# Optimization experiments

Hardware: AMD Instinct MI355X
Metric: run time of the kernel (lower is better)

## Reference

```python
import jax, jax.numpy as jnp
import numpy as np

NUM_HEADS = 1


def setup_inputs() -> dict:
    key = jax.random.key(0)
    k1, k2, k3 = jax.random.split(key, 3)
    B, C, H, W = 32, 1024, 32, 32
    x = jax.random.normal(k1, (B, C, H, W), dtype=jnp.float32)
    w_qkv = jax.random.normal(k2, (3 * C, C), dtype=jnp.float32) * (C ** -0.5)
    w_proj = jax.random.normal(k3, (C, C), dtype=jnp.float32) * (C ** -0.5)
    b_proj = jnp.zeros((C,), dtype=jnp.float32)
    return {"x": x, "w_qkv": w_qkv, "w_proj": w_proj, "b_proj": b_proj}


def reference(x, w_qkv, w_proj, b_proj):
    B, C, H, W = x.shape
    nh = NUM_HEADS
    hd = C // nh
    S = H * W
    # 1x1 conv (no bias) == channel matmul
    qkv = jnp.einsum('bchw,oc->bohw', x, w_qkv)          # [B, 3C, H, W]
    qkv = qkv.reshape(B * nh, 3 * hd, S)
    q, k, v = jnp.split(qkv, 3, axis=1)                   # each [B*nh, hd, S]
    scale = hd ** -0.25
    attn = jax.nn.softmax(
        jnp.einsum('bct,bcs->bts', q * scale, k * scale), axis=-1)  # [B*nh, S, S]
    # faithful to source einsum 'bts,bcs->bts': sums v over channel dim only
    h = attn * jnp.sum(v, axis=1, keepdims=True)          # [B*nh, S, S]
    h = h.reshape(B, nh * S, H, W)                        # requires nh*S == C
    out = jnp.einsum('bchw,oc->bohw', h, w_proj) + b_proj[None, :, None, None]
    return out + x
```

## Files before the change

### kernel.cpp

```cpp
#include <hip/hip_runtime.h>
#include <hip/hip_bf16.h>
#include <stdint.h>


typedef __attribute__((ext_vector_type(8))) short short8;
typedef __attribute__((ext_vector_type(4))) float f32x4;

__device__ __forceinline__ short f2b(float f) {
    __hip_bfloat16 h = __float2bfloat16(f);
    return *reinterpret_cast<short*>(&h);
}
__device__ __forceinline__ float b2f(short s) {
    __hip_bfloat16 h;
    *reinterpret_cast<short*>(&h) = s;
    return __bfloat162float(h);
}

#define GLOAD16(gp, lp) __builtin_amdgcn_global_load_lds(                      \
    (const __attribute__((address_space(1))) unsigned int*)(gp),               \
    (__attribute__((address_space(3))) unsigned int*)(lp), 16, 0, 0)

#define WAITV4 asm volatile("s_waitcnt vmcnt(4)" ::: "memory")
#define WAITV0 asm volatile("s_waitcnt vmcnt(0)" ::: "memory")
#define WAITL0 asm volatile("s_waitcnt lgkmcnt(0)" ::: "memory")
#define BAR()  { asm volatile("" ::: "memory"); __builtin_amdgcn_s_barrier(); \
                 asm volatile("" ::: "memory"); }

__global__ void k_wvsum(const float* __restrict__ wqkv, float* __restrict__ wvsum) {
    int c = blockIdx.x * 256 + threadIdx.x;
    int o0 = blockIdx.y * 32;
    float s = 0.f;
    const float* p = wqkv + (size_t)(2048 + o0) * 1024 + c;
    #pragma unroll 8
    for (int o = 0; o < 32; ++o) s += p[(size_t)o * 1024];
    atomicAdd(&wvsum[c], s);
}

__global__ void k_cvt(const float* __restrict__ in, short* __restrict__ out) {
    int i = (blockIdx.x * 256 + threadIdx.x) * 4;
    #pragma unroll
    for (int j = 0; j < 4; ++j) out[i + j] = f2b(in[i + j]);
}

__global__ void k_xpose(const float* __restrict__ x, const float* __restrict__ wvsum,
                        short* __restrict__ xT, float* __restrict__ vsum) {
    __shared__ float tile[32][33];
    __shared__ float ps[8][32];
    int b = blockIdx.z;
    int s0 = blockIdx.x * 32, c0 = blockIdx.y * 32;
    int tx = threadIdx.x, ty = threadIdx.y;
    const float* xb = x + ((size_t)b << 20);
    float p = 0.f;
    #pragma unroll
    for (int i = 0; i < 4; ++i) {
        int cl = ty + i * 8;
        float v = xb[(size_t)(c0 + cl) * 1024 + s0 + tx];
        tile[cl][tx] = v;
        p += v * wvsum[c0 + cl];
    }
    ps[ty][tx] = p;
    __syncthreads();
    short* xTb = xT + ((size_t)b << 20);
    #pragma unroll
    for (int i = 0; i < 4; ++i) {
        int sl = ty + i * 8;
        xTb[(size_t)(s0 + sl) * 1024 + c0 + tx] = f2b(tile[tx][sl]);
    }
    if (ty == 0) {
        float s = 0.f;
        #pragma unroll
        for (int i = 0; i < 8; ++i) s += ps[i][tx];
        atomicAdd(&vsum[b * 1024 + s0 + tx], s);
    }
}

template <int MODE, int TM, int TN>
__global__ __launch_bounds__(512, 2)
void k_gemm(const short* __restrict__ A0, size_t strideA, int lda,
            const short* __restrict__ B0, size_t strideB, int ldb,
            void* __restrict__ O0, size_t strideO, int ldo,
            float* __restrict__ Z,
            const float* __restrict__ scale,
            const float* __restrict__ bias,
            const float* __restrict__ xres) {
    __shared__ __align__(16) short As[2 * 256 * 64];
    __shared__ __align__(16) short Bs[2 * 256 * 64];

    constexpr int TPB = TM * TN;
    constexpr int CPX = TPB * 4;
    int wg = blockIdx.x;
    int swz = (wg & 7) * CPX + (wg >> 3);
    int z = swz / TPB;
    int rz = swz - z * TPB;
    int m0 = (rz / TN) * 256, n0 = (rz % TN) * 256;

    int tid = threadIdx.x;
    int wid = tid >> 6, l = tid & 63;
    int wm = wid >> 2, wn = wid & 3;
    int lr = l & 15, lg = l >> 4;

    const short* A = A0 + (size_t)z * strideA;
    const short* Bt = B0 + (size_t)z * strideB;

    int srow = wid * 16 + (l >> 3);
    int scol = ((l & 7) ^ (l >> 3)) * 8;
    const short* gA = A + (size_t)(m0 + srow) * lda + scol;
    const short* gB = Bt + (size_t)(n0 + srow) * ldb + scol;
    char* const ldsA = (char*)As;
    char* const ldsB = (char*)Bs;
    int sdst = wid * 2048;

    auto SA = [&](int buf, int h, int t) __attribute__((always_inline)) {
        const short* g = gA + (size_t)(h * 128) * lda + t * 64;
        char* d = ldsA + buf * 32768 + h * 16384 + sdst;
        GLOAD16(g, d);
        GLOAD16(g + (size_t)8 * lda, d + 1024);
    };
    auto SB = [&](int buf, int h, int t) __attribute__((always_inline)) {
        const short* g = gB + (size_t)(h * 128) * ldb + t * 64;
        char* d = ldsB + buf * 32768 + h * 16384 + sdst;
        GLOAD16(g, d);
        GLOAD16(g + (size_t)8 * ldb, d + 1024);
    };

    int cs0 = ((lg) ^ (lr & 7)) * 16;
    int cs1 = ((4 + lg) ^ (lr & 7)) * 16;
    int arow = (wm * 128 + lr) * 128;
    int brow = (wn * 64 + lr) * 128;

    short8 af[8], bf0[4], bf1[4];
    f32x4 acc[8][4] = {};

    auto RDA = [&](int buf, int mh) __attribute__((always_inline)) {
        const char* p = ldsA + buf * 32768 + arow + mh * 8192;
        #pragma unroll
        for (int mi = 0; mi < 4; ++mi) {
            af[mi * 2]     = *(const short8*)(p + mi * 2048 + cs0);
            af[mi * 2 + 1] = *(const short8*)(p + mi * 2048 + cs1);
        }
    };
    auto RDB = [&](short8* dst, int buf, int nh) __attribute__((always_inline)) {
        const char* p = ldsB + buf * 32768 + brow + nh * 4096;
        #pragma unroll
        for (int ni = 0; ni < 2; ++ni) {
            dst[ni * 2]     = *(const short8*)(p + ni * 2048 + cs0);
            dst[ni * 2 + 1] = *(const short8*)(p + ni * 2048 + cs1);
        }
    };
    auto MMA = [&](const short8* bfp, int mh, int nh) __attribute__((always_inline)) {
        __builtin_amdgcn_s_setprio(1);
        #pragma unroll
        for (int ks = 0; ks < 2; ++ks)
            #pragma unroll
            for (int mi = 0; mi < 4; ++mi)
                #pragma unroll
                for (int ni = 0; ni < 2; ++ni)
                    acc[mh * 4 + mi][nh * 2 + ni] =
                        __builtin_amdgcn_mfma_f32_16x16x32_bf16(
                            af[mi * 2 + ks], bfp[ni * 2 + ks],
                            acc[mh * 4 + mi][nh * 2 + ni], 0, 0, 0);
        __builtin_amdgcn_s_setprio(0);
    };

    SB(0, 0, 0); SB(0, 1, 0); SA(0, 0, 0); SA(0, 1, 0);
    SB(1, 0, 1); SB(1, 1, 1);
    WAITV4;
    BAR();

    for (int t = 0; t < 16; ++t) {
        int b = t & 1;
        RDA(b, 0); RDB(bf0, b, 0);
        if (t < 15) SA(b ^ 1, 0, t + 1);
        BAR(); WAITL0; MMA(bf0, 0, 0); BAR();
        RDB(bf1, b, 1);
        if (t < 15) SA(b ^ 1, 1, t + 1);
        BAR(); WAITL0; MMA(bf1, 0, 1); BAR();
        RDA(b, 1);
        if (t < 14) SB(b, 0, t + 2);
        BAR(); WAITL0; MMA(bf0, 1, 0); BAR();
        if (t < 14) SB(b, 1, t + 2);
        if (t <= 13) { WAITV4; } else if (t == 14) { WAITV0; }
        BAR(); MMA(bf1, 1, 1); BAR();
    }

    int rb = m0 + wm * 128, cb = n0 + wn * 64;
    if (MODE == 0) {
        short* O = (short*)O0 + (size_t)z * strideO;
        #pragma unroll
        for (int mi = 0; mi < 8; ++mi)
            #pragma unroll
            for (int ni = 0; ni < 4; ++ni)
                #pragma unroll
                for (int r = 0; r < 4; ++r)
                    O[(size_t)(rb + mi * 16 + lg * 4 + r) * ldo + cb + ni * 16 + lr] =
                        f2b(acc[mi][ni][r]);
    } else if (MODE == 1) {
        short* O = (short*)O0 + (size_t)z * strideO;
        float* Zb = Z + z * 1024;
        #pragma unroll
        for (int ni = 0; ni < 4; ++ni) {
            float zs = 0.f;
            #pragma unroll
            for (int mi = 0; mi < 8; ++mi)
                #pragma unroll
                for (int r = 0; r < 4; ++r) {
                    float ev = __expf(acc[mi][ni][r] * 0.03125f);
                    O[(size_t)(rb + mi * 16 + lg * 4 + r) * ldo + cb + ni * 16 + lr] = f2b(ev);
                    zs += ev;
                }
            zs += __shfl_xor(zs, 16);
            zs += __shfl_xor(zs, 32);
            if (l < 16) atomicAdd(&Zb[cb + ni * 16 + l], zs);
        }
    } else {
        float* O = (float*)O0 + (size_t)z * strideO;
        const float* xr = xres + (size_t)z * strideO;
        #pragma unroll
        for (int mi = 0; mi < 8; ++mi)
            #pragma unroll
            for (int ni = 0; ni < 4; ++ni)
                #pragma unroll
                for (int r = 0; r < 4; ++r) {
                    int row = rb + mi * 16 + lg * 4 + r;
                    int col = cb + ni * 16 + lr;
                    O[(size_t)row * ldo + col] = acc[mi][ni][r] * scale[z * 1024 + col] +
                                                 bias[row] + xr[(size_t)row * ldo + col];
                }
    }
}

__global__ void k_invz(float* Z) {
    int i = blockIdx.x * 256 + threadIdx.x;
    Z[i] = 1.0f / Z[i];
}

__global__ void k_wpscale(const short* __restrict__ wp_b, const float* __restrict__ invZ,
                          short* __restrict__ wp_s) {
    size_t i8 = ((size_t)blockIdx.x * 256 + threadIdx.x) * 8;
    int b = (int)(i8 >> 20);
    int t0 = (int)(i8 & 1023);
    short8 w = *(const short8*)&wp_b[i8 & 1048575];
    const float* iz = invZ + b * 1024 + t0;
    short8 r;
    #pragma unroll
    for (int j = 0; j < 8; ++j) r[j] = f2b(b2f(w[j]) * iz[j]);
    *(short8*)&wp_s[i8] = r;
}

extern "C" void kernel_launch(void* const* d_in, const int* in_sizes, int n_in,
                              void* d_out, int out_size, void* d_ws, size_t ws_size,
                              hipStream_t stream) {
    const float* x     = (const float*)d_in[0];
    const float* wqkv  = (const float*)d_in[1];
    const float* wproj = (const float*)d_in[2];
    const float* bproj = (const float*)d_in[3];
    float* out = (float*)d_out;

    char* ws = (char*)d_ws;
    size_t off = 0;
    auto alloc = [&](size_t bytes) {
        void* p = ws + off;
        off += (bytes + 255) & ~(size_t)255;
        return p;
    };
    float* wvsum = (float*)alloc(1024 * 4);
    short* wqk_b = (short*)alloc((size_t)2048 * 1024 * 2);
    short* wp_b  = (short*)alloc((size_t)1024 * 1024 * 2);
    short* xT    = (short*)alloc((size_t)32 * 1024 * 1024 * 2);
    short* qkT   = (short*)alloc((size_t)32 * 1024 * 2048 * 2);
    short* attnT = (short*)alloc((size_t)32 * 1024 * 1024 * 2);
    float* vsum  = (float*)alloc(32 * 1024 * 4);
    float* Zbuf  = (float*)alloc(32 * 1024 * 4);

    hipMemsetAsync(wvsum, 0, 1024 * 4, stream);
    hipMemsetAsync(vsum, 0, 32 * 1024 * 4, stream);
    hipMemsetAsync(Zbuf, 0, 32 * 1024 * 4, stream);

    k_wvsum<<<dim3(4, 32), 256, 0, stream>>>(wqkv, wvsum);
    k_cvt<<<2048, 256, 0, stream>>>(wqkv, wqk_b);
    k_cvt<<<1024, 256, 0, stream>>>(wproj, wp_b);
    k_xpose<<<dim3(32, 32, 32), dim3(32, 8), 0, stream>>>(x, wvsum, xT, vsum);

    k_gemm<0, 4, 8><<<1024, 512, 0, stream>>>(
        xT, (size_t)1048576, 1024, wqk_b, 0, 1024,
        qkT, (size_t)2097152, 2048, nullptr, nullptr, nullptr, nullptr);

    k_gemm<1, 4, 4><<<512, 512, 0, stream>>>(
        qkT + 1024, (size_t)2097152, 2048, qkT, (size_t)2097152, 2048,
        attnT, (size_t)1048576, 1024, Zbuf, nullptr, nullptr, nullptr);

    k_invz<<<128, 256, 0, stream>>>(Zbuf);

    short* wp_s = xT;
    k_wpscale<<<16384, 256, 0, stream>>>(wp_b, Zbuf, wp_s);

    k_gemm<2, 4, 4><<<512, 512, 0, stream>>>(
        wp_s, (size_t)1048576, 1024, attnT, (size_t)1048576, 1024,
        out, (size_t)1048576, 1024, nullptr, vsum, bproj, x);
}
```

Measured before the change: 436.5 us.

## Precompute Wk^T Wq product to replace the QKV GEMM with a C×C GEMM

Rewrites the scores q^T k as x^T (Wq^T Wk) x. The weight product M = Wq^T Wk is computed once as a split-K GEMM (8 fp32 partials reduced to bf16), then applied per batch to x. This replaces the 2048-wide QKV projection with a 1024-wide one and stops writing the larger qkT buffer. The GEMM also gains a templated K-iteration count with peeled prologue and epilogue iterations. The extra bf16 rounding of M and of the intermediate product may change numerics slightly.

```diff
diff --git a/kernel.cpp b/kernel.cpp
--- a/kernel.cpp
+++ b/kernel.cpp
@@ -4,6 +4,7 @@
 
 
 typedef __attribute__((ext_vector_type(8))) short short8;
+typedef __attribute__((ext_vector_type(4))) short short4_t;
 typedef __attribute__((ext_vector_type(4))) float f32x4;
 
 __device__ __forceinline__ short f2b(float f) {
@@ -74,7 +75,36 @@
     }
 }
 
-template <int MODE, int TM, int TN>
+__global__ void k_xposew(const float* __restrict__ wqkv, short* __restrict__ WT) {
+    __shared__ float tile[32][33];
+    int w = blockIdx.z;
+    int o0 = blockIdx.x * 32, c0 = blockIdx.y * 32;
+    int tx = threadIdx.x, ty = threadIdx.y;
+    const float* src = wqkv + (size_t)w * 1048576;
+    #pragma unroll
+    for (int i = 0; i < 4; ++i)
+        tile[ty + i * 8][tx] = src[(size_t)(o0 + ty + i * 8) * 1024 + c0 + tx];
+    __syncthreads();
+    short* dst = WT + (size_t)w * 1048576;
+    #pragma unroll
+    for (int i = 0; i < 4; ++i) {
+        int cl = ty + i * 8;
+        dst[(size_t)(c0 + cl) * 1024 + o0 + tx] = f2b(tile[tx][cl]);
+    }
+}
+
+__global__ void k_red8(const float* __restrict__ part, short* __restrict__ MT) {
+    int i4 = (blockIdx.x * 256 + threadIdx.x) * 4;
+    f32x4 s = *(const f32x4*)&part[i4];
+    #pragma unroll
+    for (int z = 1; z < 8; ++z) s += *(const f32x4*)&part[(size_t)z * 1048576 + i4];
+    short4_t r;
+    #pragma unroll
+    for (int j = 0; j < 4; ++j) r[j] = f2b(s[j]);
+    *(short4_t*)&MT[i4] = r;
+}
+
+template <int MODE, int TM, int TN, int NT>
 __global__ __launch_bounds__(512, 2)
 void k_gemm(const short* __restrict__ A0, size_t strideA, int lda,
             const short* __restrict__ B0, size_t strideB, int ldb,
@@ -87,9 +117,9 @@
     __shared__ __align__(16) short Bs[2 * 256 * 64];
 
     constexpr int TPB = TM * TN;
-    constexpr int CPX = TPB * 4;
     int wg = blockIdx.x;
-    int swz = (wg & 7) * CPX + (wg >> 3);
+    int cpx = gridDim.x >> 3;
+    int swz = (wg & 7) * cpx + (wg >> 3);
     int z = swz / TPB;
     int rz = swz - z * TPB;
     int m0 = (rz / TN) * 256, n0 = (rz % TN) * 256;
@@ -163,24 +193,47 @@
     };
 
     SB(0, 0, 0); SB(0, 1, 0); SA(0, 0, 0); SA(0, 1, 0);
-    SB(1, 0, 1); SB(1, 1, 1);
-    WAITV4;
+    if constexpr (NT > 1) {
+        SB(1, 0, 1); SB(1, 1, 1);
+        WAITV4;
+    } else {
+        WAITV0;
+    }
     BAR();
 
-    for (int t = 0; t < 16; ++t) {
+    #pragma unroll 2
+    for (int t = 0; t < NT - 2; ++t) {
         int b = t & 1;
+        RDA(b, 0); RDB(bf0, b, 0); SA(b ^ 1, 0, t + 1);
+        BAR(); WAITL0; MMA(bf0, 0, 0); BAR();
+        RDB(bf1, b, 1); SA(b ^ 1, 1, t + 1);
+        BAR(); WAITL0; MMA(bf1, 0, 1); BAR();
+        RDA(b, 1); SB(b, 0, t + 2);
+        BAR(); WAITL0; MMA(bf0, 1, 0); BAR();
+        SB(b, 1, t + 2); WAITV4;
+        BAR(); MMA(bf1, 1, 1); BAR();
+    }
+    if constexpr (NT > 1) {
+        constexpr int tp = NT - 2;
+        constexpr int b = tp & 1;
+        RDA(b, 0); RDB(bf0, b, 0); SA(b ^ 1, 0, NT - 1);
+        BAR(); WAITL0; MMA(bf0, 0, 0); BAR();
+        RDB(bf1, b, 1); SA(b ^ 1, 1, NT - 1);
+        BAR(); WAITL0; MMA(bf1, 0, 1); BAR();
+        RDA(b, 1);
+        BAR(); WAITL0; MMA(bf0, 1, 0); BAR();
+        WAITV0;
+        BAR(); MMA(bf1, 1, 1); BAR();
+    }
+    {
+        constexpr int b = (NT - 1) & 1;
         RDA(b, 0); RDB(bf0, b, 0);
-        if (t < 15) SA(b ^ 1, 0, t + 1);
         BAR(); WAITL0; MMA(bf0, 0, 0); BAR();
         RDB(bf1, b, 1);
-        if (t < 15) SA(b ^ 1, 1, t + 1);
         BAR(); WAITL0; MMA(bf1, 0, 1); BAR();
         RDA(b, 1);
-        if (t < 14) SB(b, 0, t + 2);
         BAR(); WAITL0; MMA(bf0, 1, 0); BAR();
-        if (t < 14) SB(b, 1, t + 2);
-        if (t <= 13) { WAITV4; } else if (t == 14) { WAITV0; }
-        BAR(); MMA(bf1, 1, 1); BAR();
+        MMA(bf1, 1, 1);
     }
 
     int rb = m0 + wm * 128, cb = n0 + wn * 64;
@@ -212,7 +265,7 @@
             zs += __shfl_xor(zs, 32);
             if (l < 16) atomicAdd(&Zb[cb + ni * 16 + l], zs);
         }
-    } else {
+    } else if (MODE == 2) {
         float* O = (float*)O0 + (size_t)z * strideO;
         const float* xr = xres + (size_t)z * strideO;
         #pragma unroll
@@ -226,6 +279,16 @@
                     O[(size_t)row * ldo + col] = acc[mi][ni][r] * scale[z * 1024 + col] +
                                                  bias[row] + xr[(size_t)row * ldo + col];
                 }
+    } else {
+        float* O = (float*)O0 + (size_t)z * strideO;
+        #pragma unroll
+        for (int mi = 0; mi < 8; ++mi)
+            #pragma unroll
+            for (int ni = 0; ni < 4; ++ni)
+                #pragma unroll
+                for (int r = 0; r < 4; ++r)
+                    O[(size_t)(rb + mi * 16 + lg * 4 + r) * ldo + cb + ni * 16 + lr] =
+                        acc[mi][ni][r];
     }
 }
 
@@ -264,10 +327,12 @@
         return p;
     };
     float* wvsum = (float*)alloc(1024 * 4);
-    short* wqk_b = (short*)alloc((size_t)2048 * 1024 * 2);
     short* wp_b  = (short*)alloc((size_t)1024 * 1024 * 2);
     short* xT    = (short*)alloc((size_t)32 * 1024 * 1024 * 2);
-    short* qkT   = (short*)alloc((size_t)32 * 1024 * 2048 * 2);
+    short* WT    = (short*)alloc((size_t)2 * 1024 * 1024 * 2);
+    float* MTp   = (float*)alloc((size_t)8 * 1024 * 1024 * 4);
+    short* MT    = (short*)alloc((size_t)1024 * 1024 * 2);
+    short* YT    = (short*)alloc((size_t)32 * 1024 * 1024 * 2);
     short* attnT = (short*)alloc((size_t)32 * 1024 * 1024 * 2);
     float* vsum  = (float*)alloc(32 * 1024 * 4);
     float* Zbuf  = (float*)alloc(32 * 1024 * 4);
@@ -277,16 +342,21 @@
     hipMemsetAsync(Zbuf, 0, 32 * 1024 * 4, stream);
 
     k_wvsum<<<dim3(4, 32), 256, 0, stream>>>(wqkv, wvsum);
-    k_cvt<<<2048, 256, 0, stream>>>(wqkv, wqk_b);
     k_cvt<<<1024, 256, 0, stream>>>(wproj, wp_b);
+    k_xposew<<<dim3(32, 32, 2), dim3(32, 8), 0, stream>>>(wqkv, WT);
     k_xpose<<<dim3(32, 32, 32), dim3(32, 8), 0, stream>>>(x, wvsum, xT, vsum);
 
-    k_gemm<0, 4, 8><<<1024, 512, 0, stream>>>(
-        xT, (size_t)1048576, 1024, wqk_b, 0, 1024,
-        qkT, (size_t)2097152, 2048, nullptr, nullptr, nullptr, nullptr);
-
-    k_gemm<1, 4, 4><<<512, 512, 0, stream>>>(
-        qkT + 1024, (size_t)2097152, 2048, qkT, (size_t)2097152, 2048,
+    k_gemm<3, 4, 4, 2><<<128, 512, 0, stream>>>(
+        WT + 1048576, (size_t)128, 1024, WT, (size_t)128, 1024,
+        MTp, (size_t)1048576, 1024, nullptr, nullptr, nullptr, nullptr);
+    k_red8<<<1024, 256, 0, stream>>>(MTp, MT);
+
+    k_gemm<0, 4, 4, 16><<<512, 512, 0, stream>>>(
+        xT, (size_t)1048576, 1024, MT, 0, 1024,
+        YT, (size_t)1048576, 1024, nullptr, nullptr, nullptr, nullptr);
+
+    k_gemm<1, 4, 4, 16><<<512, 512, 0, stream>>>(
+        xT, (size_t)1048576, 1024, YT, (size_t)1048576, 1024,
         attnT, (size_t)1048576, 1024, Zbuf, nullptr, nullptr, nullptr);
 
     k_invz<<<128, 256, 0, stream>>>(Zbuf);
@@ -294,7 +364,7 @@
     short* wp_s = xT;
     k_wpscale<<<16384, 256, 0, stream>>>(wp_b, Zbuf, wp_s);
 
-    k_gemm<2, 4, 4><<<512, 512, 0, stream>>>(
+    k_gemm<2, 4, 4, 16><<<512, 512, 0, stream>>>(
         wp_s, (size_t)1048576, 1024, attnT, (size_t)1048576, 1024,
         out, (size_t)1048576, 1024, nullptr, vsum, bproj, x);
 }
```

After: 362.7 us (median of 2 runs). 16.9% less time.
